# Kernel optimization log

Hardware: AMD Instinct MI355X
Metric: run time of the kernel (lower is better)

## Reference

```python
import jax, jax.numpy as jnp
import numpy as np

B, H, W, C = 16, 64, 64, 256
DIRECTIONS = [(0, -1), (1, -1), (1, 0), (1, 1), (0, 1), (-1, 1), (-1, 0), (-1, -1)]


def _shift(g, dx, dy):
    # zero-padded shift matching the torch _shift_grid semantics:
    # result[:, max(0,dy):H+min(0,dy), max(0,dx):W+min(0,dx)] = g[src slices]
    _, h, w, _ = g.shape
    padded = jnp.pad(g, ((0, 0), (max(0, dy), max(0, -dy)), (max(0, dx), max(0, -dx)), (0, 0)))
    return padded[:, max(0, -dy):max(0, -dy) + h, max(0, -dx):max(0, -dx) + w, :]


def setup_inputs() -> dict:
    key = jax.random.key(0)
    k1, k2, k3, k4 = jax.random.split(key, 4)
    grid_embedding = jax.random.normal(k1, (B, H, W, C), dtype=jnp.float32)
    Wd = jax.random.normal(k2, (8, C, C), dtype=jnp.float32) * 0.01  # per-direction weights
    Wc = jax.random.normal(k3, (C, 8 * C), dtype=jnp.float32) * 0.02  # Linear weight [out, in]
    bc = jax.random.normal(k4, (C,), dtype=jnp.float32) * 0.02
    return {"grid_embedding": grid_embedding, "Wd": Wd, "Wc": Wc, "bc": bc}


def reference(grid_embedding, Wd, Wc, bc):
    # stack the 8 zero-padded shifted copies: [8, B, H, W, C]
    shifted = jnp.stack([_shift(grid_embedding, dx, dy) for (dx, dy) in DIRECTIONS], axis=0)
    # per-direction channel matmul: [B, H, W, 8, C] (d-major over last two dims matches torch.cat order)
    proc = jnp.einsum('dbhwc,dce->bhwde', shifted, Wd)
    combined = proc.reshape(grid_embedding.shape[0], grid_embedding.shape[1], grid_embedding.shape[2], -1)
    # nn.Linear: y = x @ W.T + b
    return combined @ Wc.T + bc
```

## Files before the change

kernel.cpp:

```cpp
#include <hip/hip_runtime.h>


typedef unsigned short u16;
typedef unsigned int u32;
typedef __attribute__((ext_vector_type(8))) short bf16x8;
typedef __attribute__((ext_vector_type(4))) float f32x4;

#define GP_BYTES 35684352

__device__ __forceinline__ u16 f2bf(float f) {
  u32 u = __float_as_uint(f);
  u32 r = u + 0x7fffu + ((u >> 16) & 1u);
  return (u16)(r >> 16);
}
__device__ __forceinline__ u32 pack2(float a, float b) {
  return (u32)f2bf(a) | ((u32)f2bf(b) << 16);
}

__global__ __launch_bounds__(256) void pad_convert(const float* __restrict__ g,
                                                   u16* __restrict__ gp) {
  int id = blockIdx.x * 256 + threadIdx.x;
  if (id >= 2230272) return;
  int c8 = id & 31;
  int t = id >> 5;
  int xx = t % 66;
  int s = t / 66;
  int yy = s % 66;
  int b  = s / 66;
  u32 o0 = 0, o1 = 0, o2 = 0, o3 = 0;
  if (yy != 0 && yy != 65 && xx != 0 && xx != 65) {
    const float* src = g + ((((b << 6) + yy - 1) << 6) + xx - 1) * 256 + (c8 << 3);
    float4 fa = *(const float4*)src;
    float4 fb = *(const float4*)(src + 4);
    o0 = pack2(fa.x, fa.y);
    o1 = pack2(fa.z, fa.w);
    o2 = pack2(fb.x, fb.y);
    o3 = pack2(fb.z, fb.w);
  }
  uint4 v; v.x = o0; v.y = o1; v.z = o2; v.w = o3;
  *(uint4*)(gp + (size_t)id * 8) = v;
}

__global__ __launch_bounds__(256) void build_mt(const float* __restrict__ Wd,
                                                const float* __restrict__ Wc,
                                                u16* __restrict__ Bf) {
  __shared__ __align__(16) u16 As[128 * 32];
  __shared__ __align__(16) u16 Bs[128 * 32];
  const int bid = blockIdx.x;
  const int n0    = (bid & 1) << 7;
  const int mblk  = bid >> 1;
  const int d     = mblk >> 1;
  const int chalf = (mblk & 1) << 7;
  const int tid  = threadIdx.x;
  const int lane = tid & 63, wid = tid >> 6;
  const int wm = (wid >> 1) << 6, wn = (wid & 1) << 6;
  const int quad = lane >> 4, r16 = lane & 15;
  const int srow = tid >> 1, hh = tid & 1;
  const int swz  = (srow >> 1) & 3;
  const int ssl  = (quad ^ ((r16 >> 1) & 3)) << 3;
  f32x4 acc[4][4] = {};

  for (int e0 = 0; e0 < 256; e0 += 32) {
    __syncthreads();
    const float* pa = Wd + (size_t)(d * 256 + chalf + srow) * 256 + e0 + hh * 16;
    const float* pb = Wc + (size_t)(n0 + srow) * 2048 + d * 256 + e0 + hh * 16;
#pragma unroll
    for (int i = 0; i < 2; ++i) {
      float4 a0 = *(const float4*)(pa + i * 8);
      float4 a1 = *(const float4*)(pa + i * 8 + 4);
      float4 b0 = *(const float4*)(pb + i * 8);
      float4 b1 = *(const float4*)(pb + i * 8 + 4);
      uint4 va, vb;
      va.x = pack2(a0.x, a0.y); va.y = pack2(a0.z, a0.w);
      va.z = pack2(a1.x, a1.y); va.w = pack2(a1.z, a1.w);
      vb.x = pack2(b0.x, b0.y); vb.y = pack2(b0.z, b0.w);
      vb.z = pack2(b1.x, b1.y); vb.w = pack2(b1.z, b1.w);
      int slot = (2 * hh + i) ^ swz;
      *(uint4*)&As[srow * 32 + slot * 8] = va;
      *(uint4*)&Bs[srow * 32 + slot * 8] = vb;
    }
    __syncthreads();
    bf16x8 bfr[4];
#pragma unroll
    for (int nt = 0; nt < 4; ++nt)
      bfr[nt] = *(const bf16x8*)&Bs[(wn + nt * 16 + r16) * 32 + ssl];
#pragma unroll
    for (int mt = 0; mt < 4; ++mt) {
      bf16x8 af = *(const bf16x8*)&As[(wm + mt * 16 + r16) * 32 + ssl];
#pragma unroll
      for (int nt = 0; nt < 4; ++nt)
        acc[mt][nt] = __builtin_amdgcn_mfma_f32_16x16x32_bf16(af, bfr[nt], acc[mt][nt], 0, 0, 0);
    }
  }
#pragma unroll
  for (int mt = 0; mt < 4; ++mt) {
#pragma unroll
    for (int nt = 0; nt < 4; ++nt) {
      const int o = n0 + wn + nt * 16 + r16;
      f32x4 v = acc[mt][nt];
#pragma unroll
      for (int r = 0; r < 4; ++r) {
        const int c = chalf + wm + mt * 16 + quad * 4 + r;
        const int lane2 = (o & 15) + (((c >> 3) & 3) << 4);
        const size_t idx = ((size_t)((d * 8 + (c >> 5)) * 16 + (o >> 4)) * 512) + lane2 * 8 + (c & 7);
        Bf[idx] = f2bf(v[r]);
      }
    }
  }
}

__constant__ int DOFF[8] = {16896, 16640, -256, -17152, -16896, -16640, 256, 17152};

__device__ __forceinline__ void async16(const u16* g, u16* l) {
  __builtin_amdgcn_global_load_lds((const __attribute__((address_space(1))) u32*)g,
                                   (__attribute__((address_space(3))) u32*)l, 16, 0, 0);
}

__global__ __launch_bounds__(256, 4) void conv_gemm(const u16* __restrict__ gp,
                                                    const u16* __restrict__ Bf,
                                                    const float* __restrict__ bc,
                                                    float* __restrict__ out) {
  __shared__ __align__(16) u16 Asm[2][4096];
  const int bid = blockIdx.x;
  const int xcd = bid & 7;
  const int idx = bid >> 3;
  const int b   = (xcd << 1) | (idx >> 6);
  const int w   = idx & 63;
  const int y0  = (w >> 1) << 1;
  const int n0  = (w & 1) << 7;

  const int tid  = threadIdx.x;
  const int lane = tid & 63;
  const int wid  = tid >> 6;
  const int wm   = (wid >> 1) << 6;
  const int wn   = (wid & 1) << 6;
  const int quad = lane >> 4;
  const int r16  = lane & 15;

  const int arow  = tid >> 2;
  const int chunk = (tid & 3) ^ ((tid >> 3) & 3);
  const int coff  = chunk << 3;
  const u16* baseA = gp + ((b * 66 + y0 + 1) * 66 + arow + 1) * 256 + coff;
  const int ldso = tid * 8;

  const u16* baseBf = Bf + (size_t)((n0 >> 4) + (wn >> 4)) * 512 + lane * 8;

  f32x4 acc[4][4] = {};

  auto prefetchA = [&](int kt, int bi) {
    const int off = DOFF[kt >> 3] + ((kt & 7) << 5);
    async16(baseA + off,            Asm[bi] + ldso);
    async16(baseA + off + 66 * 256, Asm[bi] + 2048 + ldso);
  };

  const int ssl = (quad ^ ((r16 >> 1) & 3)) << 3;

  prefetchA(0, 0);
  prefetchA(1, 1);
  bf16x8 bcur[4];
  {
    const u16* bp = baseBf;
#pragma unroll
    for (int nt = 0; nt < 4; ++nt) bcur[nt] = *(const bf16x8*)(bp + nt * 512);
  }
  __syncthreads();

  for (int kt = 0; kt < 64; ++kt) {
    const int ktn = (kt < 63) ? kt + 1 : 63;
    const u16* bp = baseBf + (size_t)ktn * 8192;
    bf16x8 bnxt[4];
#pragma unroll
    for (int nt = 0; nt < 4; ++nt) bnxt[nt] = *(const bf16x8*)(bp + nt * 512);

    const u16* Ab = Asm[kt & 1];
#pragma unroll
    for (int mt = 0; mt < 4; ++mt) {
      bf16x8 af = *(const bf16x8*)&Ab[(wm + mt * 16 + r16) * 32 + ssl];
#pragma unroll
      for (int nt = 0; nt < 4; ++nt)
        acc[mt][nt] = __builtin_amdgcn_mfma_f32_16x16x32_bf16(af, bcur[nt], acc[mt][nt], 0, 0, 0);
    }
    __syncthreads();
    if (kt < 62) prefetchA(kt + 2, kt & 1);
#pragma unroll
    for (int nt = 0; nt < 4; ++nt) bcur[nt] = bnxt[nt];
  }

  const int pbase = (b * 64 + y0) * 64;
#pragma unroll
  for (int nt = 0; nt < 4; ++nt) {
    const int o = n0 + wn + nt * 16 + r16;
    const float bias = bc[o];
#pragma unroll
    for (int mt = 0; mt < 4; ++mt) {
      const int pr = pbase + wm + mt * 16 + quad * 4;
      f32x4 v = acc[mt][nt];
#pragma unroll
      for (int r = 0; r < 4; ++r)
        out[(size_t)(pr + r) * 256 + o] = v[r] + bias;
    }
  }
}

extern "C" void kernel_launch(void* const* d_in, const int* in_sizes, int n_in,
                              void* d_out, int out_size, void* d_ws, size_t ws_size,
                              hipStream_t stream) {
  const float* g  = (const float*)d_in[0];
  const float* Wd = (const float*)d_in[1];
  const float* Wc = (const float*)d_in[2];
  const float* bc = (const float*)d_in[3];
  float* out = (float*)d_out;
  u16* gp = (u16*)d_ws;
  u16* Bf = (u16*)((char*)d_ws + GP_BYTES);

  pad_convert<<<8712, 256, 0, stream>>>(g, gp);
  build_mt<<<32, 256, 0, stream>>>(Wd, Wc, Bf);
  conv_gemm<<<1024, 256, 0, stream>>>(gp, Bf, bc, out);
}
```

Baseline: 200.3 us.

## Deepen A-tile LDS ring to four stages with manual vmcnt waits

The conv_gemm A-tile shared buffer grows from two to four slots. Each iteration now issues the async global-to-LDS load for tile kt+2 before the MFMAs, rather than after the barrier. The full __syncthreads is replaced by an explicit s_waitcnt vmcnt(2) plus s_barrier, so the newest A prefetch can stay in flight across the barrier. The goal is more overlap between memory traffic and MFMA work, at the cost of doubling LDS per block, which may limit occupancy, and of fragile hand-counted wait values.

```diff
diff --git a/kernel.cpp b/kernel.cpp
--- a/kernel.cpp
+++ b/kernel.cpp
@@ -120,7 +120,7 @@
                                                     const u16* __restrict__ Bf,
                                                     const float* __restrict__ bc,
                                                     float* __restrict__ out) {
-  __shared__ __align__(16) u16 Asm[2][4096];
+  __shared__ __align__(16) u16 Asm[4][4096];
   const int bid = blockIdx.x;
   const int xcd = bid & 7;
   const int idx = bid >> 3;
@@ -145,45 +145,67 @@
 
   const u16* baseBf = Bf + (size_t)((n0 >> 4) + (wn >> 4)) * 512 + lane * 8;
 
+  const int ssl = (quad ^ ((r16 >> 1) & 3)) << 3;
+
   f32x4 acc[4][4] = {};
-
-  auto prefetchA = [&](int kt, int bi) {
+  bf16x8 bcur[4], bnxt[4];
+
+  auto issueA = [&](int kt) {
     const int off = DOFF[kt >> 3] + ((kt & 7) << 5);
-    async16(baseA + off,            Asm[bi] + ldso);
-    async16(baseA + off + 66 * 256, Asm[bi] + 2048 + ldso);
-  };
-
-  const int ssl = (quad ^ ((r16 >> 1) & 3)) << 3;
-
-  prefetchA(0, 0);
-  prefetchA(1, 1);
-  bf16x8 bcur[4];
+    async16(baseA + off,            Asm[kt & 3] + ldso);
+    async16(baseA + off + 66 * 256, Asm[kt & 3] + 2048 + ldso);
+  };
+  auto loadB = [&](int kt, bf16x8* dst) {
+    const u16* bp = baseBf + (size_t)kt * 8192;
+#pragma unroll
+    for (int nt = 0; nt < 4; ++nt) dst[nt] = *(const bf16x8*)(bp + nt * 512);
+  };
+  auto readA = [&](int kt, bf16x8* af) {
+    const u16* Ab = Asm[kt & 3];
+#pragma unroll
+    for (int mt = 0; mt < 4; ++mt)
+      af[mt] = *(const bf16x8*)&Ab[(wm + mt * 16 + r16) * 32 + ssl];
+  };
+  auto domfma = [&](const bf16x8* af, const bf16x8* bb) {
+#pragma unroll
+    for (int mt = 0; mt < 4; ++mt)
+#pragma unroll
+      for (int nt = 0; nt < 4; ++nt)
+        acc[mt][nt] = __builtin_amdgcn_mfma_f32_16x16x32_bf16(af[mt], bb[nt], acc[mt][nt], 0, 0, 0);
+  };
+
+  loadB(0, bcur);
+  issueA(0);
+  issueA(1);
+  asm volatile("s_waitcnt vmcnt(2)" ::: "memory");
+  asm volatile("s_barrier" ::: "memory");
+
+#pragma unroll 2
+  for (int kt = 0; kt < 62; ++kt) {
+    loadB(kt + 1, bnxt);
+    bf16x8 af[4];
+    readA(kt, af);
+    issueA(kt + 2);
+    domfma(af, bcur);
+    asm volatile("s_waitcnt vmcnt(2)" ::: "memory");
+    asm volatile("s_barrier" ::: "memory");
+#pragma unroll
+    for (int nt = 0; nt < 4; ++nt) bcur[nt] = bnxt[nt];
+  }
   {
-    const u16* bp = baseBf;
-#pragma unroll
-    for (int nt = 0; nt < 4; ++nt) bcur[nt] = *(const bf16x8*)(bp + nt * 512);
-  }
-  __syncthreads();
-
-  for (int kt = 0; kt < 64; ++kt) {
-    const int ktn = (kt < 63) ? kt + 1 : 63;
-    const u16* bp = baseBf + (size_t)ktn * 8192;
-    bf16x8 bnxt[4];
-#pragma unroll
-    for (int nt = 0; nt < 4; ++nt) bnxt[nt] = *(const bf16x8*)(bp + nt * 512);
-
-    const u16* Ab = Asm[kt & 1];
-#pragma unroll
-    for (int mt = 0; mt < 4; ++mt) {
-      bf16x8 af = *(const bf16x8*)&Ab[(wm + mt * 16 + r16) * 32 + ssl];
-#pragma unroll
-      for (int nt = 0; nt < 4; ++nt)
-        acc[mt][nt] = __builtin_amdgcn_mfma_f32_16x16x32_bf16(af, bcur[nt], acc[mt][nt], 0, 0, 0);
-    }
-    __syncthreads();
-    if (kt < 62) prefetchA(kt + 2, kt & 1);
+    loadB(63, bnxt);
+    bf16x8 af[4];
+    readA(62, af);
+    domfma(af, bcur);
+    asm volatile("s_waitcnt vmcnt(0)" ::: "memory");
+    asm volatile("s_barrier" ::: "memory");
 #pragma unroll
     for (int nt = 0; nt < 4; ++nt) bcur[nt] = bnxt[nt];
+  }
+  {
+    bf16x8 af[4];
+    readA(63, af);
+    domfma(af, bcur);
   }
 
   const int pbase = (b * 64 + y0) * 64;
```

After: 197.8 us. About the same (-1.3%).
